# Kernel optimization log

Hardware: AMD Instinct MI355X
Metric: run time of the kernel (lower is better)

Reference implementation:

```python
import jax, jax.numpy as jnp
import numpy as np


def _laplacian_kernel(x, z, bandwidth):
    x_sq = jnp.sum(x * x, axis=-1, keepdims=True)          # [N, 1]
    z_sq = jnp.sum(z * z, axis=-1)[None, :]                # [1, M]
    d2 = x_sq + z_sq - 2.0 * jnp.einsum('nd,md->nm', x, z)  # [N, M]
    d = jnp.sqrt(jnp.maximum(d2, 0.0))
    return jnp.exp(-d / bandwidth)


def setup_inputs() -> dict:
    key = jax.random.key(0)
    k1, k2, k3 = jax.random.split(key, 3)
    N, M, D, Y = 8192, 20000, 1024, 256
    batch = jax.random.normal(k1, (N, D), dtype=jnp.float32)
    centers = jax.random.normal(k2, (M, D), dtype=jnp.float32)
    weight = jax.random.normal(k3, (M, Y), dtype=jnp.float32) * 0.02
    return {"batch": batch, "centers": centers, "weight": weight, "bandwidth": 10}


def reference(batch, centers, weight, bandwidth):
    kmat = _laplacian_kernel(batch, centers, float(bandwidth))  # [N, M]
    pred = kmat @ weight                                        # [N, Y]
    return pred
```

## Files before the change

### kernel.cpp

```cpp
#include <hip/hip_runtime.h>
#include <stdint.h>

#define N_ROWS 8192
#define D_DIM  1024
#define M_CENT 20000
#define M_PAD  20224
#define M_TILES 79
#define Y_DIM  256
#define BM 64
#define BN 256
#define BK 64
#define MSPLIT 8
#define TILES_PER_SPLIT 10
#define LDSP_STRIDE 264

typedef __attribute__((ext_vector_type(4))) float  f32x4;
typedef __attribute__((ext_vector_type(8))) __bf16 bf16x8;

__device__ __forceinline__ unsigned short f2bf(float f) {
    union { float f; unsigned u; } v; v.f = f;
    unsigned u = v.u;
    u += 0x7FFFu + ((u >> 16) & 1u);
    return (unsigned short)(u >> 16);
}

__device__ __forceinline__ void gll16(void* lds, const void* g) {
    __builtin_amdgcn_global_load_lds(
        (const __attribute__((address_space(1))) void*)g,
        (__attribute__((address_space(3))) void*)lds, 16, 0, 0);
}

__global__ void cast_rows_kernel(const float* __restrict__ src,
                                 unsigned short* __restrict__ dst,
                                 float* __restrict__ sq, int nrows_valid) {
    int row = blockIdx.x;
    int t = threadIdx.x;
    float s = 0.f;
    if (row < nrows_valid) {
        float4 v = ((const float4*)(src + (size_t)row * D_DIM))[t];
        s = v.x * v.x + v.y * v.y + v.z * v.z + v.w * v.w;
        ushort4 o;
        o.x = f2bf(v.x); o.y = f2bf(v.y); o.z = f2bf(v.z); o.w = f2bf(v.w);
        ((ushort4*)(dst + (size_t)row * D_DIM))[t] = o;
    } else {
        ((ushort4*)(dst + (size_t)row * D_DIM))[t] = make_ushort4(0, 0, 0, 0);
    }
    __shared__ float red[4];
    for (int off = 32; off; off >>= 1) s += __shfl_down(s, off, 64);
    if ((t & 63) == 0) red[t >> 6] = s;
    __syncthreads();
    if (t == 0) sq[row] = red[0] + red[1] + red[2] + red[3];
}

__global__ void cast_wT_kernel(const float* __restrict__ w,
                               unsigned short* __restrict__ wT) {
    __shared__ float tile[32][33];
    int k0 = blockIdx.x * 32;
    int y0 = blockIdx.y * 32;
    int tx = threadIdx.x & 31;
    int ty = threadIdx.x >> 5;
    #pragma unroll
    for (int i = 0; i < 4; ++i) {
        int k = k0 + ty + i * 8;
        float v = (k < M_CENT) ? w[(size_t)k * Y_DIM + y0 + tx] : 0.f;
        tile[tx][ty + i * 8] = v;
    }
    __syncthreads();
    #pragma unroll
    for (int i = 0; i < 4; ++i) {
        int yl = ty + i * 8;
        wT[(size_t)(y0 + yl) * M_PAD + k0 + tx] = f2bf(tile[yl][tx]);
    }
}

__global__ void __launch_bounds__(256, 2)
fused_kernel(const unsigned short* __restrict__ Xb,
             const unsigned short* __restrict__ Zb,
             const unsigned short* __restrict__ WbT,
             const float* __restrict__ xsq,
             const float* __restrict__ zsq,
             const int* __restrict__ bwp,
             float* __restrict__ out) {
    __shared__ union {
        struct {
            unsigned short x[BM * BK];
            unsigned short z[BN * BK];
        } s1;
        unsigned short p[BM * LDSP_STRIDE];
    } lds;
    __shared__ float lds_xsq[BM];
    __shared__ float lds_zsq[BN];

    const int t    = threadIdx.x;
    const int wave = t >> 6;
    const int lane = t & 63;
    const int quad = lane >> 4;
    const int l16  = lane & 15;
    const int cx   = l16 & 7;

    const int row0 = blockIdx.x * BM;
    int mt = blockIdx.y * TILES_PER_SPLIT;
    int mt_end = mt + TILES_PER_SPLIT;
    if (mt_end > M_TILES) mt_end = M_TILES;

    int bwi = *bwp;
    float bw;
    if (bwi > 0 && bwi < 1000000) bw = (float)bwi;
    else { union { int i; float f; } u; u.i = bwi; bw = u.f; }
    const float inv_bw = 1.0f / bw;

    if (t < BM) lds_xsq[t] = xsq[row0 + t];

    const f32x4 vzero = {0.f, 0.f, 0.f, 0.f};
    f32x4 Oacc[16];
    #pragma unroll
    for (int i = 0; i < 16; ++i) Oacc[i] = vzero;

    for (; mt < mt_end; ++mt) {
        __syncthreads();

        const int m0 = mt * BN;
        lds_zsq[t] = zsq[m0 + t];

        f32x4 S[16];
        #pragma unroll
        for (int i = 0; i < 16; ++i) S[i] = vzero;

        for (int kc = 0; kc < D_DIM / BK; ++kc) {
            const int kbase = kc * BK;
            #pragma unroll
            for (int i = 0; i < 2; ++i) {
                int lin = t + i * 256;
                int row = lin >> 3, c = lin & 7;
                gll16(&lds.s1.x[lin * 8],
                      Xb + (size_t)(row0 + row) * D_DIM + kbase + ((c ^ (row & 7)) * 8));
            }
            #pragma unroll
            for (int i = 0; i < 8; ++i) {
                int lin = t + i * 256;
                int row = lin >> 3, c = lin & 7;
                gll16(&lds.s1.z[lin * 8],
                      Zb + (size_t)(m0 + row) * D_DIM + kbase + ((c ^ (row & 7)) * 8));
            }
            __syncthreads();
            #pragma unroll
            for (int kt = 0; kt < 2; ++kt) {
                const int sw = ((kt * 4 + quad) ^ cx) * 8;
                bf16x8 a[4], b[4];
                #pragma unroll
                for (int it = 0; it < 4; ++it)
                    a[it] = *(const bf16x8*)&lds.s1.x[(it * 16 + l16) * BK + sw];
                #pragma unroll
                for (int jt = 0; jt < 4; ++jt)
                    b[jt] = *(const bf16x8*)&lds.s1.z[(wave * 64 + jt * 16 + l16) * BK + sw];
                #pragma unroll
                for (int it = 0; it < 4; ++it)
                    #pragma unroll
                    for (int jt = 0; jt < 4; ++jt)
                        S[it * 4 + jt] = __builtin_amdgcn_mfma_f32_16x16x32_bf16(
                            a[it], b[jt], S[it * 4 + jt], 0, 0, 0);
            }
            __syncthreads();
        }

        #pragma unroll
        for (int it = 0; it < 4; ++it) {
            #pragma unroll
            for (int jt = 0; jt < 4; ++jt) {
                f32x4 s4 = S[it * 4 + jt];
                const int col = wave * 64 + jt * 16 + l16;
                const float zq = lds_zsq[col];
                #pragma unroll
                for (int r = 0; r < 4; ++r) {
                    const int row = it * 16 + quad * 4 + r;
                    float d2 = lds_xsq[row] + zq - 2.0f * s4[r];
                    d2 = fmaxf(d2, 0.f);
                    float p = __expf(-sqrtf(d2) * inv_bw);
                    lds.p[row * LDSP_STRIDE + col] = f2bf(p);
                }
            }
        }
        __syncthreads();

        #pragma unroll
        for (int ks = 0; ks < 8; ++ks) {
            const int koff = ks * 32 + quad * 8;
            bf16x8 a[4], b[4];
            #pragma unroll
            for (int rt = 0; rt < 4; ++rt)
                a[rt] = *(const bf16x8*)&lds.p[(rt * 16 + l16) * LDSP_STRIDE + koff];
            #pragma unroll
            for (int ct = 0; ct < 4; ++ct) {
                const int y = wave * 64 + ct * 16 + l16;
                b[ct] = *(const bf16x8*)(WbT + (size_t)y * M_PAD + m0 + koff);
            }
            #pragma unroll
            for (int rt = 0; rt < 4; ++rt)
                #pragma unroll
                for (int ct = 0; ct < 4; ++ct)
                    Oacc[rt * 4 + ct] = __builtin_amdgcn_mfma_f32_16x16x32_bf16(
                        a[rt], b[ct], Oacc[rt * 4 + ct], 0, 0, 0);
        }
    }

    #pragma unroll
    for (int rt = 0; rt < 4; ++rt) {
        #pragma unroll
        for (int ct = 0; ct < 4; ++ct) {
            f32x4 v = Oacc[rt * 4 + ct];
            const int y = wave * 64 + ct * 16 + l16;
            #pragma unroll
            for (int r = 0; r < 4; ++r) {
                const int row = row0 + rt * 16 + quad * 4 + r;
                atomicAdd(&out[(size_t)row * Y_DIM + y], v[r]);
            }
        }
    }
}

extern "C" void kernel_launch(void* const* d_in, const int* in_sizes, int n_in,
                              void* d_out, int out_size, void* d_ws, size_t ws_size,
                              hipStream_t stream) {
    const float* X = (const float*)d_in[0];
    const float* Z = (const float*)d_in[1];
    const float* W = (const float*)d_in[2];
    const int*  bw = (const int*)d_in[3];
    float* out = (float*)d_out;

    char* ws = (char*)d_ws;
    size_t off = 0;
    unsigned short* Xb  = (unsigned short*)(ws + off); off += (size_t)N_ROWS * D_DIM * 2;
    unsigned short* Zb  = (unsigned short*)(ws + off); off += (size_t)M_PAD * D_DIM * 2;
    unsigned short* WbT = (unsigned short*)(ws + off); off += (size_t)Y_DIM * M_PAD * 2;
    float* xsq = (float*)(ws + off); off += (size_t)N_ROWS * 4;
    float* zsq = (float*)(ws + off); off += (size_t)M_PAD * 4;

    hipMemsetAsync(d_out, 0, (size_t)out_size * sizeof(float), stream);
    cast_rows_kernel<<<N_ROWS, 256, 0, stream>>>(X, Xb, xsq, N_ROWS);
    cast_rows_kernel<<<M_PAD, 256, 0, stream>>>(Z, Zb, zsq, M_CENT);
    cast_wT_kernel<<<dim3(M_PAD / 32, Y_DIM / 32), 256, 0, stream>>>(W, WbT);
    fused_kernel<<<dim3(N_ROWS / BM, MSPLIT), 256, 0, stream>>>(Xb, Zb, WbT, xsq, zsq, bw, out);
}
```

Measured before the change: 746.0 us.

## Double-buffer the distance GEMM K-loop with prefetch of next chunk

Halves the K chunk to 32 and splits the X/Z LDS staging into two buffers. The async global-to-LDS loads for chunk k+1 are issued right after a barrier and overlap the MFMAs on chunk k, with one barrier per chunk instead of two. Load addresses are precomputed once per block, and the XOR swizzle on the LDS layout is dropped. Dropping the swizzle can raise LDS bank conflicts on the 64-byte row stride, and the smaller chunk does less MFMA work per barrier.

```diff
diff --git a/kernel.cpp b/kernel.cpp
--- a/kernel.cpp
+++ b/kernel.cpp
@@ -9,7 +9,8 @@
 #define Y_DIM  256
 #define BM 64
 #define BN 256
-#define BK 64
+#define BK2 32
+#define NKC (D_DIM / BK2)
 #define MSPLIT 8
 #define TILES_PER_SPLIT 10
 #define LDSP_STRIDE 264
@@ -83,8 +84,8 @@
              float* __restrict__ out) {
     __shared__ union {
         struct {
-            unsigned short x[BM * BK];
-            unsigned short z[BN * BK];
+            unsigned short x[2][BM * BK2];
+            unsigned short z[2][BN * BK2];
         } s1;
         unsigned short p[BM * LDSP_STRIDE];
     } lds;
@@ -96,7 +97,6 @@
     const int lane = t & 63;
     const int quad = lane >> 4;
     const int l16  = lane & 15;
-    const int cx   = l16 & 7;
 
     const int row0 = blockIdx.x * BM;
     int mt = blockIdx.y * TILES_PER_SPLIT;
@@ -111,6 +111,15 @@
 
     if (t < BM) lds_xsq[t] = xsq[row0 + t];
 
+    const int xrow = t >> 2, xch = t & 3;
+    const unsigned short* xsrc = Xb + (size_t)(row0 + xrow) * D_DIM + xch * 8;
+    size_t zoff[4];
+    #pragma unroll
+    for (int i = 0; i < 4; ++i) {
+        int lin = t + i * 256;
+        zoff[i] = (size_t)(lin >> 2) * D_DIM + (lin & 3) * 8;
+    }
+
     const f32x4 vzero = {0.f, 0.f, 0.f, 0.f};
     f32x4 Oacc[16];
     #pragma unroll
@@ -120,39 +129,39 @@
         __syncthreads();
 
         const int m0 = mt * BN;
+        const unsigned short* zsrc = Zb + (size_t)m0 * D_DIM;
         lds_zsq[t] = zsq[m0 + t];
 
         f32x4 S[16];
         #pragma unroll
         for (int i = 0; i < 16; ++i) S[i] = vzero;
 
-        for (int kc = 0; kc < D_DIM / BK; ++kc) {
-            const int kbase = kc * BK;
-            #pragma unroll
-            for (int i = 0; i < 2; ++i) {
-                int lin = t + i * 256;
-                int row = lin >> 3, c = lin & 7;
-                gll16(&lds.s1.x[lin * 8],
-                      Xb + (size_t)(row0 + row) * D_DIM + kbase + ((c ^ (row & 7)) * 8));
-            }
-            #pragma unroll
-            for (int i = 0; i < 8; ++i) {
-                int lin = t + i * 256;
-                int row = lin >> 3, c = lin & 7;
-                gll16(&lds.s1.z[lin * 8],
-                      Zb + (size_t)(m0 + row) * D_DIM + kbase + ((c ^ (row & 7)) * 8));
-            }
-            __syncthreads();
-            #pragma unroll
-            for (int kt = 0; kt < 2; ++kt) {
-                const int sw = ((kt * 4 + quad) ^ cx) * 8;
+        gll16(&lds.s1.x[0][t * 8], xsrc);
+        #pragma unroll
+        for (int i = 0; i < 4; ++i)
+            gll16(&lds.s1.z[0][(t + i * 256) * 8], zsrc + zoff[i]);
+
+        #pragma unroll 1
+        for (int kc2 = 0; kc2 < NKC / 2; ++kc2) {
+            #pragma unroll
+            for (int half = 0; half < 2; ++half) {
+                const int kc = kc2 * 2 + half;
+                __syncthreads();
+                if (kc < NKC - 1) {
+                    const int nb = half ^ 1;
+                    const size_t kb = (size_t)(kc + 1) * BK2;
+                    gll16(&lds.s1.x[nb][t * 8], xsrc + kb);
+                    #pragma unroll
+                    for (int i = 0; i < 4; ++i)
+                        gll16(&lds.s1.z[nb][(t + i * 256) * 8], zsrc + zoff[i] + kb);
+                }
                 bf16x8 a[4], b[4];
                 #pragma unroll
                 for (int it = 0; it < 4; ++it)
-                    a[it] = *(const bf16x8*)&lds.s1.x[(it * 16 + l16) * BK + sw];
+                    a[it] = *(const bf16x8*)&lds.s1.x[half][(it * 16 + l16) * BK2 + quad * 8];
                 #pragma unroll
                 for (int jt = 0; jt < 4; ++jt)
-                    b[jt] = *(const bf16x8*)&lds.s1.z[(wave * 64 + jt * 16 + l16) * BK + sw];
+                    b[jt] = *(const bf16x8*)&lds.s1.z[half][(wave * 64 + jt * 16 + l16) * BK2 + quad * 8];
                 #pragma unroll
                 for (int it = 0; it < 4; ++it)
                     #pragma unroll
@@ -160,8 +169,8 @@
                         S[it * 4 + jt] = __builtin_amdgcn_mfma_f32_16x16x32_bf16(
                             a[it], b[jt], S[it * 4 + jt], 0, 0, 0);
             }
-            __syncthreads();
-        }
+        }
+        __syncthreads();
 
         #pragma unroll
         for (int it = 0; it < 4; ++it) {
```

After: 884.9 us. 1.19x slower.

## Pre-pack operands into MFMA fragment layout and load directly to registers

Applied to the files above, without the earlier changes.

The cast kernels now write X, Z and W^T into 16-row panels laid out in MFMA fragment order, so each lane reads its bf16x8 operand with one contiguous 16-byte global load. The first GEMM drops LDS staging and its per-chunk barriers, reading fragments straight from global memory with a two-stage register double buffer, and z-squared values move to registers. This removes LDS traffic and barrier stalls, at the cost of no data sharing across waves in a block: each wave re-reads the X fragments from global/L2, and there are more outstanding global loads per wave.

```diff
diff --git a/kernel.cpp b/kernel.cpp
--- a/kernel.cpp
+++ b/kernel.cpp
@@ -9,10 +9,14 @@
 #define Y_DIM  256
 #define BM 64
 #define BN 256
-#define BK 64
 #define MSPLIT 8
 #define TILES_PER_SPLIT 10
 #define LDSP_STRIDE 264
+#define NKT 32
+#define PANEL_X (NKT * 512)
+#define NKT_M 632
+#define PANEL_W (NKT_M * 512)
+
 
 typedef __attribute__((ext_vector_type(4))) float  f32x4;
 typedef __attribute__((ext_vector_type(8))) __bf16 bf16x8;
@@ -24,27 +28,22 @@
     return (unsigned short)(u >> 16);
 }
 
-__device__ __forceinline__ void gll16(void* lds, const void* g) {
-    __builtin_amdgcn_global_load_lds(
-        (const __attribute__((address_space(1))) void*)g,
-        (__attribute__((address_space(3))) void*)lds, 16, 0, 0);
-}
-
-__global__ void cast_rows_kernel(const float* __restrict__ src,
+__global__ void pack_rows_kernel(const float* __restrict__ src,
                                  unsigned short* __restrict__ dst,
                                  float* __restrict__ sq, int nrows_valid) {
     int row = blockIdx.x;
     int t = threadIdx.x;
+    int p = row >> 4, m = row & 15;
     float s = 0.f;
+    ushort4 o = make_ushort4(0, 0, 0, 0);
     if (row < nrows_valid) {
         float4 v = ((const float4*)(src + (size_t)row * D_DIM))[t];
         s = v.x * v.x + v.y * v.y + v.z * v.z + v.w * v.w;
-        ushort4 o;
         o.x = f2bf(v.x); o.y = f2bf(v.y); o.z = f2bf(v.z); o.w = f2bf(v.w);
-        ((ushort4*)(dst + (size_t)row * D_DIM))[t] = o;
-    } else {
-        ((ushort4*)(dst + (size_t)row * D_DIM))[t] = make_ushort4(0, 0, 0, 0);
-    }
+    }
+    size_t obase = (size_t)p * PANEL_X + (size_t)(t >> 3) * 512
+                 + (size_t)((t >> 1) & 3) * 128 + m * 8 + (t & 1) * 4;
+    *(ushort4*)(dst + obase) = o;
     __shared__ float red[4];
     for (int off = 32; off; off >>= 1) s += __shfl_down(s, off, 64);
     if ((t & 63) == 0) red[t >> 6] = s;
@@ -52,51 +51,47 @@
     if (t == 0) sq[row] = red[0] + red[1] + red[2] + red[3];
 }
 
-__global__ void cast_wT_kernel(const float* __restrict__ w,
-                               unsigned short* __restrict__ wT) {
+__global__ void pack_wT_kernel(const float* __restrict__ w,
+                               unsigned short* __restrict__ wTp) {
     __shared__ float tile[32][33];
-    int k0 = blockIdx.x * 32;
+    int m0 = blockIdx.x * 32;
     int y0 = blockIdx.y * 32;
     int tx = threadIdx.x & 31;
     int ty = threadIdx.x >> 5;
     #pragma unroll
     for (int i = 0; i < 4; ++i) {
-        int k = k0 + ty + i * 8;
-        float v = (k < M_CENT) ? w[(size_t)k * Y_DIM + y0 + tx] : 0.f;
+        int mm = m0 + ty + i * 8;
+        float v = (mm < M_CENT) ? w[(size_t)mm * Y_DIM + y0 + tx] : 0.f;
         tile[tx][ty + i * 8] = v;
     }
     __syncthreads();
     #pragma unroll
     for (int i = 0; i < 4; ++i) {
         int yl = ty + i * 8;
-        wT[(size_t)(y0 + yl) * M_PAD + k0 + tx] = f2bf(tile[yl][tx]);
+        int p = (y0 >> 4) + (yl >> 4);
+        size_t off = (size_t)p * PANEL_W + (size_t)(m0 >> 5) * 512
+                   + (size_t)(tx >> 3) * 128 + (yl & 15) * 8 + (tx & 7);
+        wTp[off] = f2bf(tile[yl][tx]);
     }
 }
 
 __global__ void __launch_bounds__(256, 2)
-fused_kernel(const unsigned short* __restrict__ Xb,
-             const unsigned short* __restrict__ Zb,
-             const unsigned short* __restrict__ WbT,
+fused_kernel(const unsigned short* __restrict__ Xp,
+             const unsigned short* __restrict__ Zp,
+             const unsigned short* __restrict__ WTp,
              const float* __restrict__ xsq,
              const float* __restrict__ zsq,
              const int* __restrict__ bwp,
              float* __restrict__ out) {
-    __shared__ union {
-        struct {
-            unsigned short x[BM * BK];
-            unsigned short z[BN * BK];
-        } s1;
-        unsigned short p[BM * LDSP_STRIDE];
-    } lds;
+    __shared__ unsigned short lds_p[BM * LDSP_STRIDE];
     __shared__ float lds_xsq[BM];
-    __shared__ float lds_zsq[BN];
 
     const int t    = threadIdx.x;
     const int wave = t >> 6;
     const int lane = t & 63;
     const int quad = lane >> 4;
     const int l16  = lane & 15;
-    const int cx   = l16 & 7;
+    const int lane8 = lane * 8;
 
     const int row0 = blockIdx.x * BM;
     int mt = blockIdx.y * TILES_PER_SPLIT;
@@ -111,72 +106,76 @@
 
     if (t < BM) lds_xsq[t] = xsq[row0 + t];
 
+    const unsigned short* xp0 = Xp + (size_t)(row0 >> 4) * PANEL_X + lane8;
+
     const f32x4 vzero = {0.f, 0.f, 0.f, 0.f};
     f32x4 Oacc[16];
     #pragma unroll
     for (int i = 0; i < 16; ++i) Oacc[i] = vzero;
 
+    #pragma unroll 1
     for (; mt < mt_end; ++mt) {
+        const int m0 = mt * BN;
+        const unsigned short* zp0 = Zp + (size_t)(mt * 16 + wave * 4) * PANEL_X + lane8;
+
+        float zqv[4];
+        #pragma unroll
+        for (int jt = 0; jt < 4; ++jt)
+            zqv[jt] = zsq[m0 + wave * 64 + jt * 16 + l16];
+
+        f32x4 S[16];
+        #pragma unroll
+        for (int i = 0; i < 16; ++i) S[i] = vzero;
+
+        bf16x8 ae[4], be[4], ao[4], bo[4];
+        #pragma unroll
+        for (int i = 0; i < 4; ++i) {
+            ae[i] = *(const bf16x8*)(xp0 + (size_t)i * PANEL_X);
+            be[i] = *(const bf16x8*)(zp0 + (size_t)i * PANEL_X);
+        }
+        #pragma unroll 1
+        for (int kt2 = 0; kt2 < NKT / 2; ++kt2) {
+            const unsigned short* xk = xp0 + (size_t)(2 * kt2 + 1) * 512;
+            const unsigned short* zk = zp0 + (size_t)(2 * kt2 + 1) * 512;
+            #pragma unroll
+            for (int i = 0; i < 4; ++i) {
+                ao[i] = *(const bf16x8*)(xk + (size_t)i * PANEL_X);
+                bo[i] = *(const bf16x8*)(zk + (size_t)i * PANEL_X);
+            }
+            #pragma unroll
+            for (int it = 0; it < 4; ++it)
+                #pragma unroll
+                for (int jt = 0; jt < 4; ++jt)
+                    S[it * 4 + jt] = __builtin_amdgcn_mfma_f32_16x16x32_bf16(
+                        ae[it], be[jt], S[it * 4 + jt], 0, 0, 0);
+            #pragma unroll
+            for (int i = 0; i < 4; ++i) {
+                ae[i] = *(const bf16x8*)(xk + 512 + (size_t)i * PANEL_X);
+                be[i] = *(const bf16x8*)(zk + 512 + (size_t)i * PANEL_X);
+            }
+            #pragma unroll
+            for (int it = 0; it < 4; ++it)
+                #pragma unroll
+                for (int jt = 0; jt < 4; ++jt)
+                    S[it * 4 + jt] = __builtin_amdgcn_mfma_f32_16x16x32_bf16(
+                        ao[it], bo[jt], S[it * 4 + jt], 0, 0, 0);
+        }
+
         __syncthreads();
-
-        const int m0 = mt * BN;
-        lds_zsq[t] = zsq[m0 + t];
-
-        f32x4 S[16];
-        #pragma unroll
-        for (int i = 0; i < 16; ++i) S[i] = vzero;
-
-        for (int kc = 0; kc < D_DIM / BK; ++kc) {
-            const int kbase = kc * BK;
-            #pragma unroll
-            for (int i = 0; i < 2; ++i) {
-                int lin = t + i * 256;
-                int row = lin >> 3, c = lin & 7;
-                gll16(&lds.s1.x[lin * 8],
-                      Xb + (size_t)(row0 + row) * D_DIM + kbase + ((c ^ (row & 7)) * 8));
-            }
-            #pragma unroll
-            for (int i = 0; i < 8; ++i) {
-                int lin = t + i * 256;
-                int row = lin >> 3, c = lin & 7;
-                gll16(&lds.s1.z[lin * 8],
-                      Zb + (size_t)(m0 + row) * D_DIM + kbase + ((c ^ (row & 7)) * 8));
-            }
-            __syncthreads();
-            #pragma unroll
-            for (int kt = 0; kt < 2; ++kt) {
-                const int sw = ((kt * 4 + quad) ^ cx) * 8;
-                bf16x8 a[4], b[4];
-                #pragma unroll
-                for (int it = 0; it < 4; ++it)
-                    a[it] = *(const bf16x8*)&lds.s1.x[(it * 16 + l16) * BK + sw];
-                #pragma unroll
-                for (int jt = 0; jt < 4; ++jt)
-                    b[jt] = *(const bf16x8*)&lds.s1.z[(wave * 64 + jt * 16 + l16) * BK + sw];
-                #pragma unroll
-                for (int it = 0; it < 4; ++it)
-                    #pragma unroll
-                    for (int jt = 0; jt < 4; ++jt)
-                        S[it * 4 + jt] = __builtin_amdgcn_mfma_f32_16x16x32_bf16(
-                            a[it], b[jt], S[it * 4 + jt], 0, 0, 0);
-            }
-            __syncthreads();
-        }
-
         #pragma unroll
         for (int it = 0; it < 4; ++it) {
             #pragma unroll
             for (int jt = 0; jt < 4; ++jt) {
                 f32x4 s4 = S[it * 4 + jt];
                 const int col = wave * 64 + jt * 16 + l16;
-                const float zq = lds_zsq[col];
+                const float zq = zqv[jt];
                 #pragma unroll
                 for (int r = 0; r < 4; ++r) {
                     const int row = it * 16 + quad * 4 + r;
                     float d2 = lds_xsq[row] + zq - 2.0f * s4[r];
                     d2 = fmaxf(d2, 0.f);
                     float p = __expf(-sqrtf(d2) * inv_bw);
-                    lds.p[row * LDSP_STRIDE + col] = f2bf(p);
+                    lds_p[row * LDSP_STRIDE + col] = f2bf(p);
                 }
             }
         }
@@ -188,12 +187,11 @@
             bf16x8 a[4], b[4];
             #pragma unroll
             for (int rt = 0; rt < 4; ++rt)
-                a[rt] = *(const bf16x8*)&lds.p[(rt * 16 + l16) * LDSP_STRIDE + koff];
-            #pragma unroll
-            for (int ct = 0; ct < 4; ++ct) {
-                const int y = wave * 64 + ct * 16 + l16;
-                b[ct] = *(const bf16x8*)(WbT + (size_t)y * M_PAD + m0 + koff);
-            }
+                a[rt] = *(const bf16x8*)&lds_p[(rt * 16 + l16) * LDSP_STRIDE + koff];
+            #pragma unroll
+            for (int ct = 0; ct < 4; ++ct)
+                b[ct] = *(const bf16x8*)(WTp + (size_t)(wave * 4 + ct) * PANEL_W
+                                             + (size_t)(mt * 8 + ks) * 512 + lane8);
             #pragma unroll
             for (int rt = 0; rt < 4; ++rt)
                 #pragma unroll
@@ -229,15 +227,15 @@
 
     char* ws = (char*)d_ws;
     size_t off = 0;
-    unsigned short* Xb  = (unsigned short*)(ws + off); off += (size_t)N_ROWS * D_DIM * 2;
-    unsigned short* Zb  = (unsigned short*)(ws + off); off += (size_t)M_PAD * D_DIM * 2;
-    unsigned short* WbT = (unsigned short*)(ws + off); off += (size_t)Y_DIM * M_PAD * 2;
+    unsigned short* Xp  = (unsigned short*)(ws + off); off += (size_t)N_ROWS * D_DIM * 2;
+    unsigned short* Zp  = (unsigned short*)(ws + off); off += (size_t)M_PAD * D_DIM * 2;
+    unsigned short* WTp = (unsigned short*)(ws + off); off += (size_t)Y_DIM * M_PAD * 2;
     float* xsq = (float*)(ws + off); off += (size_t)N_ROWS * 4;
     float* zsq = (float*)(ws + off); off += (size_t)M_PAD * 4;
 
     hipMemsetAsync(d_out, 0, (size_t)out_size * sizeof(float), stream);
-    cast_rows_kernel<<<N_ROWS, 256, 0, stream>>>(X, Xb, xsq, N_ROWS);
-    cast_rows_kernel<<<M_PAD, 256, 0, stream>>>(Z, Zb, zsq, M_CENT);
-    cast_wT_kernel<<<dim3(M_PAD / 32, Y_DIM / 32), 256, 0, stream>>>(W, WbT);
-    fused_kernel<<<dim3(N_ROWS / BM, MSPLIT), 256, 0, stream>>>(Xb, Zb, WbT, xsq, zsq, bw, out);
-}
+    pack_rows_kernel<<<N_ROWS, 256, 0, stream>>>(X, Xp, xsq, N_ROWS);
+    pack_rows_kernel<<<M_PAD, 256, 0, stream>>>(Z, Zp, zsq, M_CENT);
+    pack_wT_kernel<<<dim3(M_PAD / 32, Y_DIM / 32), 256, 0, stream>>>(W, WTp);
+    fused_kernel<<<dim3(N_ROWS / BM, MSPLIT), 256, 0, stream>>>(Xp, Zp, WTp, xsq, zsq, bw, out);
+}
```

After: 809.6 us. 8.5% more time.
